# Kernel tuning notes

Measured on AMD Instinct MI355X. Metric: run time of the kernel, lower is better.

The kernel has to match this reference:

```python
import jax, jax.numpy as jnp
import numpy as np

DIM = 1024
NHEADS = 16
DIM_HEAD = 64
HIDDEN = NHEADS * DIM_HEAD  # 1024


def _xavier(key, fan_in, fan_out):
    limit = np.sqrt(6.0 / (fan_in + fan_out))
    return jax.random.uniform(key, (fan_in, fan_out), jnp.float32, -limit, limit)


def setup_inputs() -> dict:
    key = jax.random.key(0)
    kq, k1, k2, k3 = jax.random.split(key, 4)
    q = jax.random.normal(kq, (2, 2048, DIM), jnp.float32)
    Wq = _xavier(k1, DIM, HIDDEN)
    bq = jnp.zeros((HIDDEN,), jnp.float32)
    Wkv = _xavier(k2, DIM, 2 * HIDDEN)
    bkv = jnp.zeros((2 * HIDDEN,), jnp.float32)
    Wo = _xavier(k3, HIDDEN, DIM)
    bo = jnp.zeros((DIM,), jnp.float32)
    return {"q": q, "Wq": Wq, "bq": bq, "Wkv": Wkv, "bkv": bkv, "Wo": Wo, "bo": bo}


def reference(q, Wq, bq, Wkv, bkv, Wo, bo):
    scale = DIM_HEAD ** (-0.5)
    query = q @ Wq + bq                      # [b, s, hidden]
    kv = q @ Wkv + bkv                       # self-attention: kv from q
    key_, value = jnp.split(kv, 2, axis=-1)  # [b, s, hidden] each
    b, s, _ = query.shape
    query = query.reshape(b, s, NHEADS, DIM_HEAD)
    key_ = key_.reshape(b, s, NHEADS, DIM_HEAD)
    value = value.reshape(b, s, NHEADS, DIM_HEAD)
    scores = jnp.einsum('bqhd,bkhd->bhqk', query, key_) * scale
    attn = jax.nn.softmax(scores, axis=-1)
    out = jnp.einsum('bhqk,bkhd->bqhd', attn, value)
    out = out.reshape(b, s, HIDDEN)
    return out @ Wo + bo
```

## Files before the change

kernel.cpp:

```cpp
#include <hip/hip_runtime.h>

#define DIM 1024
#define NHEADS 16
#define DH 64
#define BATCH 2
#define SEQ 2048

typedef float f32x4 __attribute__((ext_vector_type(4)));
typedef short s16x8 __attribute__((ext_vector_type(8)));
typedef short s16x4 __attribute__((ext_vector_type(4)));

__device__ __forceinline__ short f2bf(float f) {
    union { float f; unsigned u; } v; v.f = f;
    unsigned r = v.u + 0x7fffu + ((v.u >> 16) & 1u);
    return (short)(r >> 16);
}

#if defined(__has_builtin)
#if __has_builtin(__builtin_amdgcn_cvt_pk_bf16_f32)
#define HAVE_PK_BF16 1
#endif
#endif
__device__ __forceinline__ unsigned f2bf_pk(float a, float b) {
#ifdef HAVE_PK_BF16
    typedef __bf16 bf16x2_t __attribute__((ext_vector_type(2)));
    bf16x2_t r = __builtin_amdgcn_cvt_pk_bf16_f32(a, b);
    return __builtin_bit_cast(unsigned, r);
#else
    return ((unsigned)(unsigned short)f2bf(b) << 16) | (unsigned short)f2bf(a);
#endif
}
__device__ __forceinline__ s16x4 pk4(float a, float b, float c, float d) {
    union { unsigned u[2]; s16x4 v; } x;
    x.u[0] = f2bf_pk(a, b); x.u[1] = f2bf_pk(c, d);
    return x.v;
}

#if defined(__has_builtin)
#if __has_builtin(__builtin_amdgcn_exp2f)
#define EXP2(x) __builtin_amdgcn_exp2f(x)
#endif
#endif
#ifndef EXP2
#define EXP2(x) exp2f(x)
#endif

__device__ __forceinline__ void gld16(const void* g, void* l) {
    __builtin_amdgcn_global_load_lds(
        (const __attribute__((address_space(1))) void*)g,
        (__attribute__((address_space(3))) void*)l, 16, 0, 0);
}

__global__ __launch_bounds__(256) void convert_bf16_kernel(
    const float* __restrict__ X, short* __restrict__ Y)
{
    const int i = (blockIdx.x * 256 + threadIdx.x) * 8;
    float4 a = *(const float4*)(X + i);
    float4 b = *(const float4*)(X + i + 4);
    union { unsigned u[4]; s16x8 v; } o;
    o.u[0] = f2bf_pk(a.x, a.y); o.u[1] = f2bf_pk(a.z, a.w);
    o.u[2] = f2bf_pk(b.x, b.y); o.u[3] = f2bf_pk(b.z, b.w);
    *(s16x8*)(Y + i) = o.v;
}

__global__ __launch_bounds__(256) void transpose_w_kernel(
    const float* __restrict__ Wq, const float* __restrict__ Wkv,
    const float* __restrict__ Wo, short* __restrict__ WT)
{
    const int t  = threadIdx.x;
    const int ng = blockIdx.x * 64 + (t & 63);
    const int k0 = (blockIdx.y * 4 + (t >> 6)) * 8;
    const float* W; int n, N;
    if (ng < 1024)      { W = Wq;  n = ng;        N = 1024; }
    else if (ng < 3072) { W = Wkv; n = ng - 1024; N = 2048; }
    else                { W = Wo;  n = ng - 3072; N = 1024; }
    float v[8];
#pragma unroll
    for (int j = 0; j < 8; ++j) v[j] = W[(size_t)(k0 + j) * N + n];
    union { unsigned u[4]; s16x8 s; } o;
    o.u[0] = f2bf_pk(v[0], v[1]); o.u[1] = f2bf_pk(v[2], v[3]);
    o.u[2] = f2bf_pk(v[4], v[5]); o.u[3] = f2bf_pk(v[6], v[7]);
    *(s16x8*)&WT[(size_t)ng * 1024 + k0] = o.s;
}

__global__ __launch_bounds__(256) void transpose_v_kernel(
    const short* __restrict__ QKV, short* __restrict__ VtG)
{
    const int t = threadIdx.x;
    const int tok0 = blockIdx.x * 64;
    const int h = blockIdx.y, b = blockIdx.z;
    __shared__ short L[64 * 72];
    const short* src = QKV + (size_t)(b * SEQ + tok0) * 3072 + 2048 + h * 64;
#pragma unroll
    for (int p = 0; p < 2; ++p) {
        int r = p * 32 + (t >> 3);
        *(s16x8*)&L[r * 72 + (t & 7) * 8] = *(const s16x8*)(src + (size_t)r * 3072 + (t & 7) * 8);
    }
    __syncthreads();
    short* dst = VtG + (size_t)(b * NHEADS + h) * 64 * SEQ + tok0;
#pragma unroll
    for (int p = 0; p < 2; ++p) {
        int u = p * 256 + t;
        int dv = u >> 3, c = (u & 7) * 8;
        s16x8 o;
#pragma unroll
        for (int j = 0; j < 8; ++j) o[j] = L[(c + j) * 72 + dv];
        *(s16x8*)(dst + (size_t)dv * SEQ + c) = o;
    }
}

template<int TM, bool OUT_BF16>
__global__ __launch_bounds__(256) void gemm_mfma_kernel(
    const short* __restrict__ A, const short* __restrict__ Bt,
    const float* __restrict__ bias0, const float* __restrict__ bias1, int nsplit,
    float s0, float s1, void* __restrict__ C, int M, int N)
{
    const int K = 1024;
    constexpr int NI = (TM == 128) ? 4 : 2;
    __shared__ short As[TM * 32];
    __shared__ short Bs[128 * 32];

    const int t    = threadIdx.x;
    const int wave = t >> 6;
    const int lane = t & 63;
    const int col  = lane & 15;
    const int quad = lane >> 4;
    const int m0 = blockIdx.y * TM;
    const int n0 = blockIdx.x * 128;
    const int wroff = (TM == 128) ? (wave >> 1) * 64 : 0;
    const int wcoff = (TM == 128) ? (wave & 1) * 64 : wave * 32;

    f32x4 acc[4][NI];
#pragma unroll
    for (int mi = 0; mi < 4; ++mi)
#pragma unroll
        for (int ni = 0; ni < NI; ++ni) acc[mi][ni] = (f32x4){0.f, 0.f, 0.f, 0.f};

    constexpr int RPW = TM / 4;
    const int ldrowA = wave * RPW + (lane >> 2);
    const int ldrowB = wave * 32  + (lane >> 2);
    const int ldcol  = (lane & 3) * 8;
    const short* Ag = A  + (size_t)(m0 + ldrowA) * K + ldcol;
    const short* Bg = Bt + (size_t)(n0 + ldrowB) * K + ldcol;
    short* AsW = &As[wave * RPW * 32];
    short* BsW = &Bs[wave * 1024];

    for (int k0 = 0; k0 < K; k0 += 32) {
        __syncthreads();
        gld16(Ag + k0, AsW);
        if (TM == 128) gld16(Ag + 16 * K + k0, AsW + 512);
        gld16(Bg + k0,          BsW);
        gld16(Bg + 16 * K + k0, BsW + 512);
        __syncthreads();

        s16x8 aA[4], bB[NI];
#pragma unroll
        for (int mi = 0; mi < 4; ++mi)
            aA[mi] = *(const s16x8*)&As[(wroff + 16 * mi + col) * 32 + quad * 8];
#pragma unroll
        for (int ni = 0; ni < NI; ++ni)
            bB[ni] = *(const s16x8*)&Bs[(wcoff + 16 * ni + col) * 32 + quad * 8];
#pragma unroll
        for (int mi = 0; mi < 4; ++mi)
#pragma unroll
            for (int ni = 0; ni < NI; ++ni)
                acc[mi][ni] = __builtin_amdgcn_mfma_f32_16x16x32_bf16(aA[mi], bB[ni], acc[mi][ni], 0, 0, 0);
    }

    float bias_v[NI], scale_v[NI];
#pragma unroll
    for (int ni = 0; ni < NI; ++ni) {
        int nb = n0 + wcoff + 16 * ni + col;
        bias_v[ni]  = (nb < nsplit) ? bias0[nb] : bias1[nb - nsplit];
        scale_v[ni] = (nb < nsplit) ? s0 : s1;
    }

#pragma unroll
    for (int mi = 0; mi < 4; ++mi)
#pragma unroll
        for (int ni = 0; ni < NI; ++ni)
#pragma unroll
            for (int r = 0; r < 4; ++r) {
                const int gm = m0 + wroff + 16 * mi + quad * 4 + r;
                const int gn = n0 + wcoff + 16 * ni + col;
                float v = (acc[mi][ni][r] + bias_v[ni]) * scale_v[ni];
                if (OUT_BF16) ((short*)C)[(size_t)gm * N + gn] = f2bf(v);
                else          ((float*)C)[(size_t)gm * N + gn] = v;
            }
}

__global__ __launch_bounds__(512) void attn_v6_kernel(
    const short* __restrict__ QKV,
    const short* __restrict__ VtG,
    short* __restrict__ O)
{
    const int qt = blockIdx.x;
    const int h  = blockIdx.y;
    const int b  = blockIdx.z;
    const int t  = threadIdx.x;
    const int wave = t >> 6;
    const int lane = t & 63;
    const int col  = lane & 15;
    const int quad = lane >> 4;
    const int wq = wave & 3;
    const int kh = wave >> 2;

    __shared__ short Ks[2][64 * 72];
    __shared__ short Vt[2][64 * 72];
    __shared__ short Ps[8][64 * 40];

    const short* Qg = QKV + (size_t)(b * SEQ + qt * 256) * 3072 + h * DH;
    const short* Kg = QKV + (size_t)(b * SEQ) * 3072 + 1024 + h * DH;
    const short* VtRow = VtG + (size_t)(b * NHEADS + h) * 64 * SEQ;

    s16x8 aQ[4][2];
#pragma unroll
    for (int tq = 0; tq < 4; ++tq)
#pragma unroll
        for (int kq = 0; kq < 2; ++kq)
            aQ[tq][kq] = *(const s16x8*)(Qg + (size_t)(wq * 64 + 16 * tq + col) * 3072 + kq * 32 + quad * 8);

    f32x4 oa[4][4];
    float lsum[4] = {0.f, 0.f, 0.f, 0.f};
#pragma unroll
    for (int td = 0; td < 4; ++td)
#pragma unroll
        for (int tq = 0; tq < 4; ++tq) oa[td][tq] = (f32x4){0.f, 0.f, 0.f, 0.f};

    const int srow = t >> 3;
    const int sc8  = (t & 7) * 8;
    const short* KgS  = Kg + (size_t)srow * 3072 + sc8;
    const short* VtgS = VtRow + (size_t)srow * SEQ + sc8;
    s16x8 kx = *(const s16x8*)KgS;
    s16x8 vx = *(const s16x8*)VtgS;

    short* PsW = &Ps[wave][0];

    for (int kt = 0; kt < SEQ / 64; ++kt) {
        const int cur = kt & 1;
        *(s16x8*)&Ks[cur][srow * 72 + sc8] = kx;
        *(s16x8*)&Vt[cur][srow * 72 + sc8] = vx;
        {
            int nt = (kt + 1 < SEQ / 64) ? kt + 1 : kt;
            kx = *(const s16x8*)(KgS + (size_t)nt * 64 * 3072);
            vx = *(const s16x8*)(VtgS + (size_t)nt * 64);
        }
        __syncthreads();

        s16x8 aK[2][2];
#pragma unroll
        for (int tk = 0; tk < 2; ++tk)
#pragma unroll
            for (int kq = 0; kq < 2; ++kq)
                aK[tk][kq] = *(const s16x8*)&Ks[cur][(kh * 32 + 16 * tk + col) * 72 + kq * 32 + quad * 8];
        f32x4 st[2][4];
#pragma unroll
        for (int tk = 0; tk < 2; ++tk)
#pragma unroll
            for (int tq = 0; tq < 4; ++tq) {
                f32x4 a = (f32x4){0.f, 0.f, 0.f, 0.f};
                a = __builtin_amdgcn_mfma_f32_16x16x32_bf16(aK[tk][0], aQ[tq][0], a, 0, 0, 0);
                a = __builtin_amdgcn_mfma_f32_16x16x32_bf16(aK[tk][1], aQ[tq][1], a, 0, 0, 0);
                st[tk][tq] = a;
            }

#pragma unroll
        for (int tk = 0; tk < 2; ++tk)
#pragma unroll
            for (int tq = 0; tq < 4; ++tq) {
                float p0 = EXP2(st[tk][tq][0]);
                float p1 = EXP2(st[tk][tq][1]);
                float p2 = EXP2(st[tk][tq][2]);
                float p3 = EXP2(st[tk][tq][3]);
                lsum[tq] += (p0 + p1) + (p2 + p3);
                *(s16x4*)&PsW[(16 * tq + col) * 40 + 16 * tk + quad * 4] = pk4(p0, p1, p2, p3);
            }
        asm volatile("s_waitcnt lgkmcnt(0)" ::: "memory");

        s16x8 bP[4];
#pragma unroll
        for (int tq = 0; tq < 4; ++tq)
            bP[tq] = *(const s16x8*)&PsW[(16 * tq + col) * 40 + quad * 8];
#pragma unroll
        for (int td = 0; td < 4; ++td) {
            const int dv = 16 * td + col;
            s16x8 aV = *(const s16x8*)&Vt[cur][dv * 72 + kh * 32 + quad * 8];
#pragma unroll
            for (int tq = 0; tq < 4; ++tq)
                oa[td][tq] = __builtin_amdgcn_mfma_f32_16x16x32_bf16(aV, bP[tq], oa[td][tq], 0, 0, 0);
        }
    }

#pragma unroll
    for (int tq = 0; tq < 4; ++tq) {
        lsum[tq] += __shfl_xor(lsum[tq], 16);
        lsum[tq] += __shfl_xor(lsum[tq], 32);
    }

    __syncthreads();
    float* red  = (float*)&Ps[0][0];
    float* redl = red + 8192;
#pragma unroll
    for (int round = 0; round < 2; ++round) {
        if (wave >= 4 && ((wave >> 1) & 1) == round) {
            const int slot = wave & 1;
#pragma unroll
            for (int td = 0; td < 4; ++td)
#pragma unroll
                for (int tq = 0; tq < 4; ++tq)
#pragma unroll
                    for (int r = 0; r < 4; ++r)
                        red[slot * 4096 + (16 * td + quad * 4 + r) * 64 + 16 * tq + col] = oa[td][tq][r];
            if (quad == 0)
#pragma unroll
                for (int tq = 0; tq < 4; ++tq)
                    redl[slot * 64 + 16 * tq + col] = lsum[tq];
        }
        __syncthreads();
        if (wave < 4 && ((wave >> 1) & 1) == round) {
            const int slot = wave & 1;
#pragma unroll
            for (int td = 0; td < 4; ++td)
#pragma unroll
                for (int tq = 0; tq < 4; ++tq)
#pragma unroll
                    for (int r = 0; r < 4; ++r)
                        oa[td][tq][r] += red[slot * 4096 + (16 * td + quad * 4 + r) * 64 + 16 * tq + col];
#pragma unroll
            for (int tq = 0; tq < 4; ++tq)
                lsum[tq] += redl[slot * 64 + 16 * tq + col];
        }
        __syncthreads();
    }

    if (wave < 4) {
        short* Og = O + (size_t)(b * SEQ + qt * 256 + wq * 64) * DIM + h * DH;
        float inv[4];
#pragma unroll
        for (int tq = 0; tq < 4; ++tq) inv[tq] = 1.f / lsum[tq];
#pragma unroll
        for (int td = 0; td < 4; ++td)
#pragma unroll
            for (int tq = 0; tq < 4; ++tq)
                *(s16x4*)(Og + (size_t)(16 * tq + col) * DIM + 16 * td + quad * 4) =
                    pk4(oa[td][tq][0] * inv[tq], oa[td][tq][1] * inv[tq],
                        oa[td][tq][2] * inv[tq], oa[td][tq][3] * inv[tq]);
    }
}

extern "C" void kernel_launch(void* const* d_in, const int* in_sizes, int n_in,
                              void* d_out, int out_size, void* d_ws, size_t ws_size,
                              hipStream_t stream)
{
    const float* q   = (const float*)d_in[0];
    const float* Wq  = (const float*)d_in[1];
    const float* bq  = (const float*)d_in[2];
    const float* Wkv = (const float*)d_in[3];
    const float* bkv = (const float*)d_in[4];
    const float* Wo  = (const float*)d_in[5];
    const float* bo  = (const float*)d_in[6];
    float* out = (float*)d_out;

    const int M = BATCH * SEQ;

    short* qb     = (short*)d_ws;
    short* WT     = qb     + (size_t)M * DIM;
    short* QKVbuf = WT     + (size_t)4096 * DIM;
    short* AObuf  = QKVbuf + (size_t)M * 3 * DIM;
    short* VtG    = (short*)d_out;

    const float QSCALE = 0.18033688011112042f;

    convert_bf16_kernel<<<(M * DIM) / (256 * 8), 256, 0, stream>>>(q, qb);
    transpose_w_kernel<<<dim3(64, 32), 256, 0, stream>>>(Wq, Wkv, Wo, WT);

    gemm_mfma_kernel<128, true><<<dim3(3 * DIM / 128, M / 128), 256, 0, stream>>>(
        qb, WT, bq, bkv, DIM, QSCALE, 1.0f, QKVbuf, M, 3 * DIM);
    transpose_v_kernel<<<dim3(SEQ / 64, NHEADS, BATCH), 256, 0, stream>>>(QKVbuf, VtG);
    attn_v6_kernel<<<dim3(SEQ / 256, NHEADS, BATCH), 512, 0, stream>>>(QKVbuf, VtG, AObuf);
    gemm_mfma_kernel<64, false><<<dim3(DIM / 128, M / 64), 256, 0, stream>>>(
        AObuf, WT + (size_t)3072 * 1024, bo, bo, 1 << 30, 1.0f, 1.0f, out, M, DIM);
}
```

Baseline: 199.0 us.

## Halve attention query tile per block to raise occupancy and add MFMA priority

The attention kernel now handles 128 query rows per block instead of 256, so each wave carries half the accumulators and the grid doubles. Shared memory is packed into one smaller buffer and launch bounds request 4 blocks per CU to raise occupancy. The two-round cross-wave reduction becomes a single round, and s_setprio wraps the MFMA sections to favour matrix issue. The cost is that each K/V tile is loaded from global memory by twice as many blocks, and each block amortises its staging over fewer MFMAs.

```diff
diff --git a/kernel.cpp b/kernel.cpp
--- a/kernel.cpp
+++ b/kernel.cpp
@@ -189,7 +189,7 @@
             }
 }
 
-__global__ __launch_bounds__(512) void attn_v6_kernel(
+__global__ __launch_bounds__(512, 4) void attn_v7_kernel(
     const short* __restrict__ QKV,
     const short* __restrict__ VtG,
     short* __restrict__ O)
@@ -205,27 +205,28 @@
     const int wq = wave & 3;
     const int kh = wave >> 2;
 
-    __shared__ short Ks[2][64 * 72];
-    __shared__ short Vt[2][64 * 72];
-    __shared__ short Ps[8][64 * 40];
-
-    const short* Qg = QKV + (size_t)(b * SEQ + qt * 256) * 3072 + h * DH;
+    __shared__ __align__(16) short L[28672];
+    short* KsB = L;
+    short* VtB = L + 2 * 64 * 72;
+    short* PsW = L + 4 * 64 * 72 + wave * (32 * 40);
+
+    const short* Qg = QKV + (size_t)(b * SEQ + qt * 128) * 3072 + h * DH;
     const short* Kg = QKV + (size_t)(b * SEQ) * 3072 + 1024 + h * DH;
     const short* VtRow = VtG + (size_t)(b * NHEADS + h) * 64 * SEQ;
 
-    s16x8 aQ[4][2];
-#pragma unroll
-    for (int tq = 0; tq < 4; ++tq)
+    s16x8 aQ[2][2];
+#pragma unroll
+    for (int tq = 0; tq < 2; ++tq)
 #pragma unroll
         for (int kq = 0; kq < 2; ++kq)
-            aQ[tq][kq] = *(const s16x8*)(Qg + (size_t)(wq * 64 + 16 * tq + col) * 3072 + kq * 32 + quad * 8);
-
-    f32x4 oa[4][4];
-    float lsum[4] = {0.f, 0.f, 0.f, 0.f};
+            aQ[tq][kq] = *(const s16x8*)(Qg + (size_t)(wq * 32 + 16 * tq + col) * 3072 + kq * 32 + quad * 8);
+
+    f32x4 oa[4][2];
+    float lsum[2] = {0.f, 0.f};
 #pragma unroll
     for (int td = 0; td < 4; ++td)
 #pragma unroll
-        for (int tq = 0; tq < 4; ++tq) oa[td][tq] = (f32x4){0.f, 0.f, 0.f, 0.f};
+        for (int tq = 0; tq < 2; ++tq) oa[td][tq] = (f32x4){0.f, 0.f, 0.f, 0.f};
 
     const int srow = t >> 3;
     const int sc8  = (t & 7) * 8;
@@ -234,12 +235,10 @@
     s16x8 kx = *(const s16x8*)KgS;
     s16x8 vx = *(const s16x8*)VtgS;
 
-    short* PsW = &Ps[wave][0];
-
     for (int kt = 0; kt < SEQ / 64; ++kt) {
         const int cur = kt & 1;
-        *(s16x8*)&Ks[cur][srow * 72 + sc8] = kx;
-        *(s16x8*)&Vt[cur][srow * 72 + sc8] = vx;
+        *(s16x8*)&KsB[cur * 4608 + srow * 72 + sc8] = kx;
+        *(s16x8*)&VtB[cur * 4608 + srow * 72 + sc8] = vx;
         {
             int nt = (kt + 1 < SEQ / 64) ? kt + 1 : kt;
             kx = *(const s16x8*)(KgS + (size_t)nt * 64 * 3072);
@@ -252,22 +251,24 @@
         for (int tk = 0; tk < 2; ++tk)
 #pragma unroll
             for (int kq = 0; kq < 2; ++kq)
-                aK[tk][kq] = *(const s16x8*)&Ks[cur][(kh * 32 + 16 * tk + col) * 72 + kq * 32 + quad * 8];
-        f32x4 st[2][4];
+                aK[tk][kq] = *(const s16x8*)&KsB[cur * 4608 + (kh * 32 + 16 * tk + col) * 72 + kq * 32 + quad * 8];
+        f32x4 st[2][2];
+        __builtin_amdgcn_s_setprio(1);
 #pragma unroll
         for (int tk = 0; tk < 2; ++tk)
 #pragma unroll
-            for (int tq = 0; tq < 4; ++tq) {
+            for (int tq = 0; tq < 2; ++tq) {
                 f32x4 a = (f32x4){0.f, 0.f, 0.f, 0.f};
                 a = __builtin_amdgcn_mfma_f32_16x16x32_bf16(aK[tk][0], aQ[tq][0], a, 0, 0, 0);
                 a = __builtin_amdgcn_mfma_f32_16x16x32_bf16(aK[tk][1], aQ[tq][1], a, 0, 0, 0);
                 st[tk][tq] = a;
             }
+        __builtin_amdgcn_s_setprio(0);
 
 #pragma unroll
         for (int tk = 0; tk < 2; ++tk)
 #pragma unroll
-            for (int tq = 0; tq < 4; ++tq) {
+            for (int tq = 0; tq < 2; ++tq) {
                 float p0 = EXP2(st[tk][tq][0]);
                 float p1 = EXP2(st[tk][tq][1]);
                 float p2 = EXP2(st[tk][tq][2]);
@@ -277,71 +278,67 @@
             }
         asm volatile("s_waitcnt lgkmcnt(0)" ::: "memory");
 
-        s16x8 bP[4];
-#pragma unroll
-        for (int tq = 0; tq < 4; ++tq)
+        s16x8 bP[2];
+#pragma unroll
+        for (int tq = 0; tq < 2; ++tq)
             bP[tq] = *(const s16x8*)&PsW[(16 * tq + col) * 40 + quad * 8];
+        __builtin_amdgcn_s_setprio(1);
 #pragma unroll
         for (int td = 0; td < 4; ++td) {
             const int dv = 16 * td + col;
-            s16x8 aV = *(const s16x8*)&Vt[cur][dv * 72 + kh * 32 + quad * 8];
-#pragma unroll
-            for (int tq = 0; tq < 4; ++tq)
+            s16x8 aV = *(const s16x8*)&VtB[cur * 4608 + dv * 72 + kh * 32 + quad * 8];
+#pragma unroll
+            for (int tq = 0; tq < 2; ++tq)
                 oa[td][tq] = __builtin_amdgcn_mfma_f32_16x16x32_bf16(aV, bP[tq], oa[td][tq], 0, 0, 0);
         }
-    }
-
-#pragma unroll
-    for (int tq = 0; tq < 4; ++tq) {
+        __builtin_amdgcn_s_setprio(0);
+    }
+
+#pragma unroll
+    for (int tq = 0; tq < 2; ++tq) {
         lsum[tq] += __shfl_xor(lsum[tq], 16);
         lsum[tq] += __shfl_xor(lsum[tq], 32);
     }
 
     __syncthreads();
-    float* red  = (float*)&Ps[0][0];
-    float* redl = red + 8192;
-#pragma unroll
-    for (int round = 0; round < 2; ++round) {
-        if (wave >= 4 && ((wave >> 1) & 1) == round) {
-            const int slot = wave & 1;
-#pragma unroll
-            for (int td = 0; td < 4; ++td)
-#pragma unroll
-                for (int tq = 0; tq < 4; ++tq)
-#pragma unroll
-                    for (int r = 0; r < 4; ++r)
-                        red[slot * 4096 + (16 * td + quad * 4 + r) * 64 + 16 * tq + col] = oa[td][tq][r];
-            if (quad == 0)
-#pragma unroll
-                for (int tq = 0; tq < 4; ++tq)
-                    redl[slot * 64 + 16 * tq + col] = lsum[tq];
+    float* red  = (float*)L;
+    float* redl = red + 4 * 64 * 36;
+    if (wave >= 4) {
+        const int slot = wave & 3;
+#pragma unroll
+        for (int td = 0; td < 4; ++td)
+#pragma unroll
+            for (int tq = 0; tq < 2; ++tq)
+#pragma unroll
+                for (int r = 0; r < 4; ++r)
+                    red[slot * 2304 + (16 * td + quad * 4 + r) * 36 + 16 * tq + col] = oa[td][tq][r];
+        if (quad == 0)
+#pragma unroll
+            for (int tq = 0; tq < 2; ++tq)
+                redl[slot * 32 + 16 * tq + col] = lsum[tq];
+    }
+    __syncthreads();
+
+    if (wave < 4) {
+        const int slot = wq;
+#pragma unroll
+        for (int td = 0; td < 4; ++td)
+#pragma unroll
+            for (int tq = 0; tq < 2; ++tq)
+#pragma unroll
+                for (int r = 0; r < 4; ++r)
+                    oa[td][tq][r] += red[slot * 2304 + (16 * td + quad * 4 + r) * 36 + 16 * tq + col];
+        float inv[2];
+#pragma unroll
+        for (int tq = 0; tq < 2; ++tq) {
+            lsum[tq] += redl[slot * 32 + 16 * tq + col];
+            inv[tq] = 1.f / lsum[tq];
         }
-        __syncthreads();
-        if (wave < 4 && ((wave >> 1) & 1) == round) {
-            const int slot = wave & 1;
-#pragma unroll
-            for (int td = 0; td < 4; ++td)
-#pragma unroll
-                for (int tq = 0; tq < 4; ++tq)
-#pragma unroll
-                    for (int r = 0; r < 4; ++r)
-                        oa[td][tq][r] += red[slot * 4096 + (16 * td + quad * 4 + r) * 64 + 16 * tq + col];
-#pragma unroll
-            for (int tq = 0; tq < 4; ++tq)
-                lsum[tq] += redl[slot * 64 + 16 * tq + col];
-        }
-        __syncthreads();
-    }
-
-    if (wave < 4) {
-        short* Og = O + (size_t)(b * SEQ + qt * 256 + wq * 64) * DIM + h * DH;
-        float inv[4];
-#pragma unroll
-        for (int tq = 0; tq < 4; ++tq) inv[tq] = 1.f / lsum[tq];
+        short* Og = O + (size_t)(b * SEQ + qt * 128 + wq * 32) * DIM + h * DH;
 #pragma unroll
         for (int td = 0; td < 4; ++td)
 #pragma unroll
-            for (int tq = 0; tq < 4; ++tq)
+            for (int tq = 0; tq < 2; ++tq)
                 *(s16x4*)(Og + (size_t)(16 * tq + col) * DIM + 16 * td + quad * 4) =
                     pk4(oa[td][tq][0] * inv[tq], oa[td][tq][1] * inv[tq],
                         oa[td][tq][2] * inv[tq], oa[td][tq][3] * inv[tq]);
@@ -377,7 +374,7 @@
     gemm_mfma_kernel<128, true><<<dim3(3 * DIM / 128, M / 128), 256, 0, stream>>>(
         qb, WT, bq, bkv, DIM, QSCALE, 1.0f, QKVbuf, M, 3 * DIM);
     transpose_v_kernel<<<dim3(SEQ / 64, NHEADS, BATCH), 256, 0, stream>>>(QKVbuf, VtG);
-    attn_v6_kernel<<<dim3(SEQ / 256, NHEADS, BATCH), 512, 0, stream>>>(QKVbuf, VtG, AObuf);
+    attn_v7_kernel<<<dim3(SEQ / 128, NHEADS, BATCH), 512, 0, stream>>>(QKVbuf, VtG, AObuf);
     gemm_mfma_kernel<64, false><<<dim3(DIM / 128, M / 64), 256, 0, stream>>>(
         AObuf, WT + (size_t)3072 * 1024, bo, bo, 1 << 30, 1.0f, 1.0f, out, M, DIM);
 }
```

Result: no change. 199.7 us (+0.4%).
